# Optimization experiments

Measured on AMD Instinct MI355X. Metric: run time of the kernel, lower is better.

Reference implementation:

```python
import jax, jax.numpy as jnp
import numpy as np

NUM_SAMPLES = 10000  # hardcoded in the torch module
BATCH, K = 512, 16


def setup_inputs() -> dict:
    key = jax.random.key(0)
    k1, k2 = jax.random.split(key)
    mean = jax.random.normal(k1, (BATCH, K), dtype=jnp.float32)
    var = jax.random.uniform(k2, (BATCH, K), dtype=jnp.float32)  # variances must be >= 0
    return {"mean": mean, "var": var}


def reference(mean, var):
    # z ~ N(0,1), shape (*, K, S); fixed key => deterministic MC draw
    z = jax.random.normal(jax.random.key(42), (*mean.shape, NUM_SAMPLES), dtype=mean.dtype)
    # affine transform to N(mean, var) samples
    sample = z * jnp.sqrt(var)[..., None] + mean[..., None]
    # softmax over the category axis K (dim=-2), per MC sample
    softmax_out = jax.nn.softmax(sample, axis=-2)
    out_mean = jnp.mean(softmax_out, axis=-1)
    # torch.var defaults to unbiased (correction=1)
    out_var = jnp.var(softmax_out, axis=-1, ddof=1)
    return out_mean, out_var
```

## Files before the change

kernel.cpp:

```cpp
#include <hip/hip_runtime.h>
#include <cstdint>
#include <math.h>


typedef float f32x2 __attribute__((ext_vector_type(2)));

#define NSAMP 10000
#define HALF_N 40960000u
#define THREADS 256
#define WAVES (THREADS / 64)
#define SPLIT 4
#define CHUNK (NSAMP / SPLIT)
#define WS_NEEDED (256 * SPLIT * 64 * sizeof(float))

#define LOG2E 1.44269504088896340736f
#define NLN2 -0.69314718055994530942f
#define SQRT_LN2 0.83255461115769775635f

__device__ __forceinline__ uint32_t rotl32(uint32_t x, int r) {
    return (x << r) | (x >> (32 - r));
}

__device__ __forceinline__ void tf2x32(uint32_t x0, uint32_t x1,
                                       uint32_t& o0, uint32_t& o1) {
    const uint32_t ks1 = 42u;
    const uint32_t ks2 = 0x1BD11BDAu ^ 42u;
    x1 += ks1;
#define TF_R(r) { x0 += x1; x1 = rotl32(x1, r); x1 ^= x0; }
    TF_R(13) TF_R(15) TF_R(26) TF_R(6)   x0 += ks1; x1 += ks2 + 1u;
    TF_R(17) TF_R(29) TF_R(16) TF_R(24)  x0 += ks2; x1 += 2u;
    TF_R(13) TF_R(15) TF_R(26) TF_R(6)                x1 += ks1 + 3u;
    TF_R(17) TF_R(29) TF_R(16) TF_R(24)  x0 += ks1; x1 += ks2 + 4u;
    TF_R(13) TF_R(15) TF_R(26) TF_R(6)   x0 += ks2; x1 += 5u;
#undef TF_R
    o0 = x0;
    o1 = x1;
}

__device__ __forceinline__ f32x2 u2_from_bits(uint32_t ba, uint32_t bb) {
    f32x2 f;
    f.x = __uint_as_float((ba >> 9) | 0x3F800000u);
    f.y = __uint_as_float((bb >> 9) | 0x3F800000u);
    f = f - (f32x2){1.0f, 1.0f};
    return __builtin_elementwise_fma(f, (f32x2){2.0f, 2.0f},
                                     (f32x2){-0.99999994f, -0.99999994f});
}

__device__ __forceinline__ f32x2 erfinv2(f32x2 x) {
    f32x2 t = __builtin_elementwise_fma(-x, x, (f32x2){1.0f, 1.0f});
    f32x2 l;
    l.x = __builtin_amdgcn_logf(t.x);
    l.y = __builtin_amdgcn_logf(t.y);
    f32x2 wm = __builtin_elementwise_fma((f32x2){NLN2, NLN2}, l,
                                         (f32x2){-2.5f, -2.5f});
#define P9(P, W, C) P = __builtin_elementwise_fma(P, W, (f32x2){C, C});
    f32x2 p1 = {2.81022636e-08f, 2.81022636e-08f};
    P9(p1, wm, 3.43273939e-07f)
    P9(p1, wm, -3.5233877e-06f)
    P9(p1, wm, -4.39150654e-06f)
    P9(p1, wm, 0.00021858087f)
    P9(p1, wm, -0.00125372503f)
    P9(p1, wm, -0.00417768164f)
    P9(p1, wm, 0.246640727f)
    P9(p1, wm, 1.50140941f)
    f32x2 sq;
    sq.x = __builtin_amdgcn_sqrtf(-l.x);
    sq.y = __builtin_amdgcn_sqrtf(-l.y);
    f32x2 wt = __builtin_elementwise_fma((f32x2){SQRT_LN2, SQRT_LN2}, sq,
                                         (f32x2){-3.0f, -3.0f});
    f32x2 p2 = {-0.000200214257f, -0.000200214257f};
    P9(p2, wt, 0.000100950558f)
    P9(p2, wt, 0.00134934322f)
    P9(p2, wt, -0.00367342844f)
    P9(p2, wt, 0.00573950773f)
    P9(p2, wt, -0.0076224613f)
    P9(p2, wt, 0.00943887047f)
    P9(p2, wt, 1.00167406f)
    P9(p2, wt, 2.83297682f)
#undef P9
    f32x2 p;
    p.x = (l.x > -7.2134752f) ? p1.x : p2.x;
    p.y = (l.y > -7.2134752f) ? p1.y : p2.y;
    return p * x;
}

__device__ __forceinline__ float wave_sum(float v) {
    v += __shfl_down(v, 32);
    v += __shfl_down(v, 16);
    v += __shfl_down(v, 8);
    v += __shfl_down(v, 4);
    v += __shfl_down(v, 2);
    v += __shfl_down(v, 1);
    return v;
}

__device__ __forceinline__ void sg_accumulate(const float* __restrict__ mean,
                                              const float* __restrict__ var,
                                              int b, int s_begin, int s_end,
                                              float (*s_mu)[16], float (*s_sv)[16],
                                              float* s_red, float* s_fin) {
    const int tid = threadIdx.x;

    if (tid < 32) {
        int h = tid >> 4, k = tid & 15;
        int bg = b + 256 * h;
        s_mu[h][k] = LOG2E * mean[bg * 16 + k];
        s_sv[h][k] = (LOG2E * 1.41421356237309515f) * sqrtf(var[bg * 16 + k]);
    }
    __syncthreads();

    f32x2 accs0[8], accq0[8], accs1[8], accq1[8];
#pragma unroll
    for (int kp = 0; kp < 8; kp++) {
        accs0[kp] = (f32x2){0.f, 0.f}; accq0[kp] = (f32x2){0.f, 0.f};
        accs1[kp] = (f32x2){0.f, 0.f}; accq1[kp] = (f32x2){0.f, 0.f};
    }

    const uint32_t base_bk = (uint32_t)(b * 16) * 10000u;

    for (int s = s_begin + tid; s < s_end; s += THREADS) {
        f32x2 e0[8], e1[8];
#pragma unroll
        for (int kp = 0; kp < 8; kp++) {
            uint32_t ia = base_bk + (uint32_t)(kp * 20000) + (uint32_t)s;
            uint32_t ib = ia + 10000u;
            uint32_t a0, a1, b0, b1;
            tf2x32(ia, ia + HALF_N, a0, a1);
            tf2x32(ib, ib + HALF_N, b0, b1);
            f32x2 z0 = erfinv2(u2_from_bits(a0, b0));
            f32x2 z1 = erfinv2(u2_from_bits(a1, b1));
            f32x2 mu0 = *(const f32x2*)&s_mu[0][2 * kp];
            f32x2 sv0 = *(const f32x2*)&s_sv[0][2 * kp];
            f32x2 mu1 = *(const f32x2*)&s_mu[1][2 * kp];
            f32x2 sv1 = *(const f32x2*)&s_sv[1][2 * kp];
            e0[kp] = __builtin_elementwise_fma(z0, sv0, mu0);
            e1[kp] = __builtin_elementwise_fma(z1, sv1, mu1);
        }
        f32x2 sm0 = {0.f, 0.f}, sm1 = {0.f, 0.f};
#pragma unroll
        for (int kp = 0; kp < 8; kp++) {
            f32x2 t0, t1;
            t0.x = __builtin_amdgcn_exp2f(e0[kp].x);
            t0.y = __builtin_amdgcn_exp2f(e0[kp].y);
            t1.x = __builtin_amdgcn_exp2f(e1[kp].x);
            t1.y = __builtin_amdgcn_exp2f(e1[kp].y);
            e0[kp] = t0; sm0 += t0;
            e1[kp] = t1; sm1 += t1;
        }
        float inv0 = __builtin_amdgcn_rcpf(sm0.x + sm0.y);
        float inv1 = __builtin_amdgcn_rcpf(sm1.x + sm1.y);
        f32x2 iv0 = {inv0, inv0}, iv1 = {inv1, inv1};
#pragma unroll
        for (int kp = 0; kp < 8; kp++) {
            f32x2 p0 = e0[kp] * iv0;
            f32x2 p1 = e1[kp] * iv1;
            accs0[kp] += p0;
            accq0[kp] = __builtin_elementwise_fma(p0, p0, accq0[kp]);
            accs1[kp] += p1;
            accq1[kp] = __builtin_elementwise_fma(p1, p1, accq1[kp]);
        }
    }

    const int lane = tid & 63, wave = tid >> 6;
#pragma unroll
    for (int kp = 0; kp < 8; kp++) {
#define RED(val, slot) { float r_ = wave_sum(val); if (lane == 0) s_red[wave * 64 + (slot)] = r_; }
        RED(accs0[kp].x, (2 * kp) * 4 + 0)
        RED(accq0[kp].x, (2 * kp) * 4 + 1)
        RED(accs1[kp].x, (2 * kp) * 4 + 2)
        RED(accq1[kp].x, (2 * kp) * 4 + 3)
        RED(accs0[kp].y, (2 * kp + 1) * 4 + 0)
        RED(accq0[kp].y, (2 * kp + 1) * 4 + 1)
        RED(accs1[kp].y, (2 * kp + 1) * 4 + 2)
        RED(accq1[kp].y, (2 * kp + 1) * 4 + 3)
#undef RED
    }
    __syncthreads();

    if (tid < 64) {
        float t = 0.f;
#pragma unroll
        for (int w = 0; w < WAVES; w++) t += s_red[w * 64 + tid];
        s_fin[tid] = t;
    }
    __syncthreads();
}

__global__ __launch_bounds__(THREADS, 4)
void sg_partial(const float* __restrict__ mean, const float* __restrict__ var,
                float* __restrict__ ws) {
    __shared__ __attribute__((aligned(8))) float s_mu[2][16];
    __shared__ __attribute__((aligned(8))) float s_sv[2][16];
    __shared__ float s_red[WAVES * 64], s_fin[64];
    const int b = blockIdx.x >> 2;
    const int chunk = blockIdx.x & 3;
    sg_accumulate(mean, var, b, chunk * CHUNK, (chunk + 1) * CHUNK,
                  s_mu, s_sv, s_red, s_fin);
    if (threadIdx.x < 64) ws[blockIdx.x * 64 + threadIdx.x] = s_fin[threadIdx.x];
}

__global__ __launch_bounds__(256)
void sg_finalize(const float* __restrict__ ws, float* __restrict__ out) {
    int t = blockIdx.x * blockDim.x + threadIdx.x;
    if (t >= 8192) return;
    int k = t & 15, h = (t >> 4) & 1, b = t >> 5;
    float sum = 0.f, sq = 0.f;
#pragma unroll
    for (int c = 0; c < SPLIT; c++) {
        const float* p = ws + ((b * SPLIT + c) * 64 + k * 4 + 2 * h);
        sum += p[0];
        sq += p[1];
    }
    float mu = sum * (1.0f / 10000.0f);
    float vr = (sq - sum * mu) * (1.0f / 9999.0f);
    int bg = b + 256 * h;
    out[bg * 16 + k] = mu;
    out[8192 + bg * 16 + k] = vr;
}

__global__ __launch_bounds__(THREADS, 4)
void sg_kernel(const float* __restrict__ mean, const float* __restrict__ var,
               float* __restrict__ out) {
    __shared__ __attribute__((aligned(8))) float s_mu[2][16];
    __shared__ __attribute__((aligned(8))) float s_sv[2][16];
    __shared__ float s_red[WAVES * 64], s_fin[64];
    const int b = blockIdx.x;
    sg_accumulate(mean, var, b, 0, NSAMP, s_mu, s_sv, s_red, s_fin);
    const int tid = threadIdx.x;
    if (tid < 32) {
        int h = tid >> 4, k = tid & 15;
        float sum = s_fin[k * 4 + 2 * h + 0];
        float sq  = s_fin[k * 4 + 2 * h + 1];
        float mu = sum * (1.0f / 10000.0f);
        float vr = (sq - sum * mu) * (1.0f / 9999.0f);
        int bg = b + 256 * h;
        out[bg * 16 + k] = mu;
        out[8192 + bg * 16 + k] = vr;
    }
}

extern "C" void kernel_launch(void* const* d_in, const int* in_sizes, int n_in,
                              void* d_out, int out_size, void* d_ws, size_t ws_size,
                              hipStream_t stream) {
    const float* mean = (const float*)d_in[0];
    const float* var  = (const float*)d_in[1];
    float* out = (float*)d_out;
    if (ws_size >= WS_NEEDED) {
        float* ws = (float*)d_ws;
        sg_partial<<<256 * SPLIT, THREADS, 0, stream>>>(mean, var, ws);
        sg_finalize<<<32, 256, 0, stream>>>(ws, out);
    } else {
        sg_kernel<<<256, THREADS, 0, stream>>>(mean, var, out);
    }
}
```

Before: 155.6 us.

## Split categories across 4-lane quads and raise sample split to 8 chunks

```diff
diff --git a/kernel.cpp b/kernel.cpp
--- a/kernel.cpp
+++ b/kernel.cpp
@@ -8,10 +8,7 @@
 #define NSAMP 10000
 #define HALF_N 40960000u
 #define THREADS 256
-#define WAVES (THREADS / 64)
-#define SPLIT 4
-#define CHUNK (NSAMP / SPLIT)
-#define WS_NEEDED (256 * SPLIT * 64 * sizeof(float))
+#define WAVES 4
 
 #define LOG2E 1.44269504088896340736f
 #define NLN2 -0.69314718055994530942f
@@ -84,13 +81,16 @@
     return p * x;
 }
 
-__device__ __forceinline__ float wave_sum(float v) {
-    v += __shfl_down(v, 32);
-    v += __shfl_down(v, 16);
-    v += __shfl_down(v, 8);
-    v += __shfl_down(v, 4);
-    v += __shfl_down(v, 2);
-    v += __shfl_down(v, 1);
+__device__ __forceinline__ float qsum4(float v) {
+    v += __shfl_xor(v, 1);
+    v += __shfl_xor(v, 2);
+    return v;
+}
+__device__ __forceinline__ float xsum16(float v) {
+    v += __shfl_xor(v, 4);
+    v += __shfl_xor(v, 8);
+    v += __shfl_xor(v, 16);
+    v += __shfl_xor(v, 32);
     return v;
 }
 
@@ -109,71 +109,76 @@
     }
     __syncthreads();
 
-    f32x2 accs0[8], accq0[8], accs1[8], accq1[8];
-#pragma unroll
-    for (int kp = 0; kp < 8; kp++) {
-        accs0[kp] = (f32x2){0.f, 0.f}; accq0[kp] = (f32x2){0.f, 0.f};
-        accs1[kp] = (f32x2){0.f, 0.f}; accq1[kp] = (f32x2){0.f, 0.f};
-    }
-
-    const uint32_t base_bk = (uint32_t)(b * 16) * 10000u;
-
-    for (int s = s_begin + tid; s < s_end; s += THREADS) {
-        f32x2 e0[8], e1[8];
-#pragma unroll
-        for (int kp = 0; kp < 8; kp++) {
-            uint32_t ia = base_bk + (uint32_t)(kp * 20000) + (uint32_t)s;
+    const int a4 = (tid & 3) * 4;
+    const int sgrp = tid >> 2;
+
+    f32x2 mu0[2], sv0[2], mu1[2], sv1[2];
+#pragma unroll
+    for (int p = 0; p < 2; p++) {
+        mu0[p] = *(const f32x2*)&s_mu[0][a4 + 2 * p];
+        sv0[p] = *(const f32x2*)&s_sv[0][a4 + 2 * p];
+        mu1[p] = *(const f32x2*)&s_mu[1][a4 + 2 * p];
+        sv1[p] = *(const f32x2*)&s_sv[1][a4 + 2 * p];
+    }
+
+    f32x2 as0[2], aq0[2], as1[2], aq1[2];
+#pragma unroll
+    for (int p = 0; p < 2; p++) {
+        as0[p] = (f32x2){0.f, 0.f}; aq0[p] = (f32x2){0.f, 0.f};
+        as1[p] = (f32x2){0.f, 0.f}; aq1[p] = (f32x2){0.f, 0.f};
+    }
+
+    const uint32_t base = (uint32_t)((b * 16 + a4) * 10000);
+
+    for (int s = s_begin + sgrp; s < s_end; s += 64) {
+        f32x2 e0[2], e1[2];
+#pragma unroll
+        for (int p = 0; p < 2; p++) {
+            uint32_t ia = base + (uint32_t)(p * 20000) + (uint32_t)s;
             uint32_t ib = ia + 10000u;
             uint32_t a0, a1, b0, b1;
             tf2x32(ia, ia + HALF_N, a0, a1);
             tf2x32(ib, ib + HALF_N, b0, b1);
             f32x2 z0 = erfinv2(u2_from_bits(a0, b0));
             f32x2 z1 = erfinv2(u2_from_bits(a1, b1));
-            f32x2 mu0 = *(const f32x2*)&s_mu[0][2 * kp];
-            f32x2 sv0 = *(const f32x2*)&s_sv[0][2 * kp];
-            f32x2 mu1 = *(const f32x2*)&s_mu[1][2 * kp];
-            f32x2 sv1 = *(const f32x2*)&s_sv[1][2 * kp];
-            e0[kp] = __builtin_elementwise_fma(z0, sv0, mu0);
-            e1[kp] = __builtin_elementwise_fma(z1, sv1, mu1);
-        }
-        f32x2 sm0 = {0.f, 0.f}, sm1 = {0.f, 0.f};
-#pragma unroll
-        for (int kp = 0; kp < 8; kp++) {
-            f32x2 t0, t1;
-            t0.x = __builtin_amdgcn_exp2f(e0[kp].x);
-            t0.y = __builtin_amdgcn_exp2f(e0[kp].y);
-            t1.x = __builtin_amdgcn_exp2f(e1[kp].x);
-            t1.y = __builtin_amdgcn_exp2f(e1[kp].y);
-            e0[kp] = t0; sm0 += t0;
-            e1[kp] = t1; sm1 += t1;
-        }
-        float inv0 = __builtin_amdgcn_rcpf(sm0.x + sm0.y);
-        float inv1 = __builtin_amdgcn_rcpf(sm1.x + sm1.y);
+            e0[p] = __builtin_elementwise_fma(z0, sv0[p], mu0[p]);
+            e1[p] = __builtin_elementwise_fma(z1, sv1[p], mu1[p]);
+        }
+#pragma unroll
+        for (int p = 0; p < 2; p++) {
+            e0[p].x = __builtin_amdgcn_exp2f(e0[p].x);
+            e0[p].y = __builtin_amdgcn_exp2f(e0[p].y);
+            e1[p].x = __builtin_amdgcn_exp2f(e1[p].x);
+            e1[p].y = __builtin_amdgcn_exp2f(e1[p].y);
+        }
+        f32x2 q0 = e0[0] + e0[1];
+        f32x2 q1 = e1[0] + e1[1];
+        float r0 = qsum4(q0.x + q0.y);
+        float r1 = qsum4(q1.x + q1.y);
+        float inv0 = __builtin_amdgcn_rcpf(r0);
+        float inv1 = __builtin_amdgcn_rcpf(r1);
         f32x2 iv0 = {inv0, inv0}, iv1 = {inv1, inv1};
 #pragma unroll
-        for (int kp = 0; kp < 8; kp++) {
-            f32x2 p0 = e0[kp] * iv0;
-            f32x2 p1 = e1[kp] * iv1;
-            accs0[kp] += p0;
-            accq0[kp] = __builtin_elementwise_fma(p0, p0, accq0[kp]);
-            accs1[kp] += p1;
-            accq1[kp] = __builtin_elementwise_fma(p1, p1, accq1[kp]);
+        for (int p = 0; p < 2; p++) {
+            f32x2 p0 = e0[p] * iv0;
+            f32x2 p1 = e1[p] * iv1;
+            as0[p] += p0; aq0[p] = __builtin_elementwise_fma(p0, p0, aq0[p]);
+            as1[p] += p1; aq1[p] = __builtin_elementwise_fma(p1, p1, aq1[p]);
         }
     }
 
     const int lane = tid & 63, wave = tid >> 6;
-#pragma unroll
-    for (int kp = 0; kp < 8; kp++) {
-#define RED(val, slot) { float r_ = wave_sum(val); if (lane == 0) s_red[wave * 64 + (slot)] = r_; }
-        RED(accs0[kp].x, (2 * kp) * 4 + 0)
-        RED(accq0[kp].x, (2 * kp) * 4 + 1)
-        RED(accs1[kp].x, (2 * kp) * 4 + 2)
-        RED(accq1[kp].x, (2 * kp) * 4 + 3)
-        RED(accs0[kp].y, (2 * kp + 1) * 4 + 0)
-        RED(accq0[kp].y, (2 * kp + 1) * 4 + 1)
-        RED(accs1[kp].y, (2 * kp + 1) * 4 + 2)
-        RED(accq1[kp].y, (2 * kp + 1) * 4 + 3)
-#undef RED
+    float vals[16] = { as0[0].x, aq0[0].x, as1[0].x, aq1[0].x,
+                       as0[0].y, aq0[0].y, as1[0].y, aq1[0].y,
+                       as0[1].x, aq0[1].x, as1[1].x, aq1[1].x,
+                       as0[1].y, aq0[1].y, as1[1].y, aq1[1].y };
+#pragma unroll
+    for (int i = 0; i < 16; i++) {
+        float r = xsum16(vals[i]);
+        if (lane < 4) {
+            int k = lane * 4 + (i >> 2);
+            s_red[wave * 64 + k * 4 + (i & 3)] = r;
+        }
     }
     __syncthreads();
 
@@ -186,28 +191,28 @@
     __syncthreads();
 }
 
+template <int NCH>
 __global__ __launch_bounds__(THREADS, 4)
 void sg_partial(const float* __restrict__ mean, const float* __restrict__ var,
                 float* __restrict__ ws) {
     __shared__ __attribute__((aligned(8))) float s_mu[2][16];
     __shared__ __attribute__((aligned(8))) float s_sv[2][16];
     __shared__ float s_red[WAVES * 64], s_fin[64];
-    const int b = blockIdx.x >> 2;
-    const int chunk = blockIdx.x & 3;
-    sg_accumulate(mean, var, b, chunk * CHUNK, (chunk + 1) * CHUNK,
-                  s_mu, s_sv, s_red, s_fin);
+    const int b = blockIdx.x / NCH;
+    const int chunk = blockIdx.x % NCH;
+    const int c0 = chunk * (NSAMP / NCH);
+    sg_accumulate(mean, var, b, c0, c0 + NSAMP / NCH, s_mu, s_sv, s_red, s_fin);
     if (threadIdx.x < 64) ws[blockIdx.x * 64 + threadIdx.x] = s_fin[threadIdx.x];
 }
 
 __global__ __launch_bounds__(256)
-void sg_finalize(const float* __restrict__ ws, float* __restrict__ out) {
+void sg_finalize(const float* __restrict__ ws, float* __restrict__ out, int nch) {
     int t = blockIdx.x * blockDim.x + threadIdx.x;
     if (t >= 8192) return;
     int k = t & 15, h = (t >> 4) & 1, b = t >> 5;
     float sum = 0.f, sq = 0.f;
-#pragma unroll
-    for (int c = 0; c < SPLIT; c++) {
-        const float* p = ws + ((b * SPLIT + c) * 64 + k * 4 + 2 * h);
+    for (int c = 0; c < nch; c++) {
+        const float* p = ws + ((b * nch + c) * 64 + k * 4 + 2 * h);
         sum += p[0];
         sq += p[1];
     }
@@ -245,10 +250,13 @@
     const float* mean = (const float*)d_in[0];
     const float* var  = (const float*)d_in[1];
     float* out = (float*)d_out;
-    if (ws_size >= WS_NEEDED) {
-        float* ws = (float*)d_ws;
-        sg_partial<<<256 * SPLIT, THREADS, 0, stream>>>(mean, var, ws);
-        sg_finalize<<<32, 256, 0, stream>>>(ws, out);
+    float* ws = (float*)d_ws;
+    if (ws_size >= 256 * 8 * 64 * sizeof(float)) {
+        sg_partial<8><<<256 * 8, THREADS, 0, stream>>>(mean, var, ws);
+        sg_finalize<<<32, 256, 0, stream>>>(ws, out, 8);
+    } else if (ws_size >= 256 * 4 * 64 * sizeof(float)) {
+        sg_partial<4><<<256 * 4, THREADS, 0, stream>>>(mean, var, ws);
+        sg_finalize<<<32, 256, 0, stream>>>(ws, out, 4);
     } else {
         sg_kernel<<<256, THREADS, 0, stream>>>(mean, var, out);
     }
```

Result: no change. 157.3 us (+1.1%).
